# Kernel optimization log

Measured on AMD Instinct MI355X. Metric: run time of the kernel, lower is better.

The kernel has to match this reference:

```python
import jax, jax.numpy as jnp
import numpy as np

B, N, D = 4, 256, 128
HID = 128
IN_DIM = 4 * D + 4  # h_i, h_j, |h_i-h_j|, h_i*h_j + 2 base + 2 completion feats


def setup_inputs() -> dict:
    key = jax.random.key(0)
    k1, k2, k3, k4, k5, k6, k7 = jax.random.split(key, 7)
    node_latents = jax.random.normal(k1, (B, N, D), dtype=jnp.float32)
    base_edge_logits = jax.random.normal(k2, (B, N, N), dtype=jnp.float32)
    completion_logits = jax.random.normal(k3, (B, N, N), dtype=jnp.float32)
    # MLP params (build_mlp: Linear(in,hid) -> ReLU -> Linear(hid,1) for num_layers=2)
    s1 = 1.0 / np.sqrt(IN_DIM)
    s2 = 1.0 / np.sqrt(HID)
    W1 = jax.random.uniform(k4, (IN_DIM, HID), minval=-s1, maxval=s1, dtype=jnp.float32)
    b1 = jax.random.uniform(k5, (HID,), minval=-s1, maxval=s1, dtype=jnp.float32)
    W2 = jax.random.uniform(k6, (HID, 1), minval=-s2, maxval=s2, dtype=jnp.float32)
    b2 = jax.random.uniform(k7, (1,), minval=-s2, maxval=s2, dtype=jnp.float32)
    return {"node_latents": node_latents, "base_edge_logits": base_edge_logits,
            "completion_logits": completion_logits, "W1": W1, "b1": b1, "W2": W2, "b2": b2}


def reference(node_latents, base_edge_logits, completion_logits, W1, b1, W2, b2):
    bsz, num_nodes, hidden_dim = node_latents.shape
    h_i = jnp.broadcast_to(node_latents[:, :, None, :], (bsz, num_nodes, num_nodes, hidden_dim))
    h_j = jnp.broadcast_to(node_latents[:, None, :, :], (bsz, num_nodes, num_nodes, hidden_dim))
    base = jnp.clip(base_edge_logits, -20.0, 20.0)
    comp = jnp.clip(completion_logits, -20.0, 20.0)
    pair_feat = jnp.concatenate([
        h_i, h_j, jnp.abs(h_i - h_j), h_i * h_j,
        base[..., None], jax.nn.sigmoid(base)[..., None],
        comp[..., None], jax.nn.sigmoid(comp)[..., None],
    ], axis=-1)  # [B, N, N, IN_DIM]
    hdn = jax.nn.relu(jnp.einsum('bijf,fh->bijh', pair_feat, W1) + b1)
    logits = (jnp.einsum('bijh,ho->bijo', hdn, W2) + b2)[..., 0]  # [B, N, N]
    logits = 0.5 * (logits + jnp.swapaxes(logits, 1, 2))
    diag = jnp.eye(num_nodes, dtype=bool)[None]
    return jnp.where(diag, jnp.float32(-1e9), logits)
```

## Files before the change

kernel.cpp:

```cpp
#include <hip/hip_runtime.h>
#include <cstdint>


typedef float f32x4 __attribute__((ext_vector_type(4)));
typedef short bf16x8 __attribute__((ext_vector_type(8)));

#define INV256 0.00390625f

__device__ __forceinline__ uint32_t pk4(float a, float b, float c, float d) {
  uint32_t u = __builtin_amdgcn_cvt_pk_fp8_f32(a, b, 0, false);
  u = __builtin_amdgcn_cvt_pk_fp8_f32(c, d, u, true);
  return u;
}
__device__ __forceinline__ uint32_t pkbf2(float lo, float hi) {
  uint32_t l = __builtin_bit_cast(uint32_t, lo);
  uint32_t h = __builtin_bit_cast(uint32_t, hi);
  return (l >> 16) | (h & 0xffff0000u);
}
__device__ __forceinline__ uint32_t rnebf(float x) {
  uint32_t u = __builtin_bit_cast(uint32_t, x);
  return (u + 0x7fffu + ((u >> 16) & 1u)) >> 16;
}
__device__ __forceinline__ uint32_t pkbf2r(float lo, float hi) {
  return rnebf(lo) | (rnebf(hi) << 16);
}
__device__ __forceinline__ float ulo(uint32_t u) {
  return __builtin_bit_cast(float, u << 16);
}
__device__ __forceinline__ float uhi(uint32_t u) {
  return __builtin_bit_cast(float, u & 0xffff0000u);
}
__device__ __forceinline__ long mk64(uint32_t lo, uint32_t hi) {
  return (long)((((unsigned long long)hi) << 32) | lo);
}
__device__ __forceinline__ bf16x8 mkbf8(uint32_t a, uint32_t b, uint32_t c, uint32_t d) {
  uint4 u;
  u.x = a; u.y = b; u.z = c; u.w = d;
  return __builtin_bit_cast(bf16x8, u);
}

__global__ __launch_bounds__(128) void pre_k(const float* __restrict__ node,
                                             const float* __restrict__ W1,
                                             const float* __restrict__ b1,
                                             float* __restrict__ PiB,
                                             float* __restrict__ Pjf,
                                             uint32_t* __restrict__ W1f8) {
  int bid = blockIdx.x;
  int tid = threadIdx.x;
  if (bid < 32) {
    int ks = bid >> 2, nip = (bid >> 1) & 1, wn = bid & 1;
    int lane = tid & 63, nilow = tid >> 6;
    int quad = lane >> 4, col = lane & 15;
    int h = wn * 64 + (nip * 2 + nilow) * 16 + col;
    int k0 = ks * 32 + quad * 8;
    float w[8];
#pragma unroll
    for (int t = 0; t < 8; ++t) w[t] = W1[(256 + k0 + t) * 128 + h] * 256.0f;
    uint2 u;
    u.x = pk4(w[0], w[1], w[2], w[3]);
    u.y = pk4(w[4], w[5], w[6], w[7]);
    reinterpret_cast<uint2*>(W1f8)[(bid * 64 + lane) * 2 + nilow] = u;
  } else {
    __shared__ float sN[128];
    int row = bid - 32;
    int h = tid;
    sN[h] = node[row * 128 + h];
    __syncthreads();
    float ai = 0.f, aj = 0.f;
#pragma unroll 8
    for (int d = 0; d < 128; ++d) {
      float v = sN[d];
      ai = fmaf(v, W1[d * 128 + h], ai);
      aj = fmaf(v, W1[(128 + d) * 128 + h], aj);
    }
    PiB[row * 128 + h] = 256.0f * (ai + b1[h]);
    Pjf[row * 128 + h] = 256.0f * aj;
  }
}

__global__ __launch_bounds__(256, 5) void main_k(
    const float* __restrict__ node, const float* __restrict__ baseL,
    const float* __restrict__ compL, const float* __restrict__ W1,
    const float* __restrict__ W2, const float* __restrict__ b2,
    const uint32_t* __restrict__ W1f8, const float* __restrict__ PiB,
    const float* __restrict__ Pjf, float* __restrict__ out) {
  __shared__ __align__(16) char smem[16384 + 8448 + 1024];
  char* sF = smem;
  uint32_t* sPP = reinterpret_cast<uint32_t*>(smem + 16384);
  uint4* sScal = reinterpret_cast<uint4*>(smem + 16384 + 8448);
  float* sP = reinterpret_cast<float*>(smem);

  const int tid = threadIdx.x;
  const int bx = blockIdx.x;
  const int b = bx / 528;
  const int t = bx - b * 528;
  int tI = (int)((65.0f - sqrtf(4225.0f - 8.0f * (float)t)) * 0.5f);
  tI = (tI < 0) ? 0 : (tI > 31 ? 31 : tI);
  while (((65 * tI - tI * tI) >> 1) > t) --tI;
  while (tI < 31 && ((65 * (tI + 1) - (tI + 1) * (tI + 1)) >> 1) <= t) ++tI;
  const int tJ = tI + (t - ((65 * tI - tI * tI) >> 1));
  const int I0 = tI * 8, J0 = tJ * 8;
  const int rowB = b * 256;

  const int lane = tid & 63;
  const int wn2 = tid >> 6;
  const int col = lane & 15, quad = lane >> 4;

  const int uB = ((wn2 & 1) << 1) | (wn2 >> 1);
  uint4 gB[8];
#pragma unroll
  for (int ks = 0; ks < 8; ++ks)
    gB[ks] = reinterpret_cast<const uint4*>(W1f8)[(ks * 4 + uB) * 64 + lane];

#pragma unroll
  for (int it = 0; it < 2; ++it) {
    int fidx = it * 256 + tid;
    int row = fidx >> 5, d4 = fidx & 31;
    int gr = rowB + ((row < 8) ? (I0 + row) : (J0 + row - 8));
    float4 a = reinterpret_cast<const float4*>(PiB + (size_t)gr * 128)[d4];
    float4 c = reinterpret_cast<const float4*>(Pjf + (size_t)gr * 128)[d4];
    uint4 u;
    u.x = pkbf2(a.x, c.x);
    u.y = pkbf2(a.y, c.y);
    u.z = pkbf2(a.z, c.z);
    u.w = pkbf2(a.w, c.w);
    *reinterpret_cast<uint4*>(&sPP[row * 132 + d4 * 4]) = u;
  }

  if (tid < 128) {
    int p = tid & 63, dir = tid >> 6;
    int iN = I0 + (p >> 3), jN = J0 + (p & 7);
    int rr = dir ? jN : iN, cc = dir ? iN : jN;
    float bl = fminf(fmaxf(baseL[(size_t)(rowB + rr) * 256 + cc], -20.f), 20.f);
    float cl = fminf(fmaxf(compL[(size_t)(rowB + rr) * 256 + cc], -20.f), 20.f);
    uint2 u;
    u.x = pkbf2(256.f * bl, 256.f / (1.f + __expf(-bl)));
    u.y = pkbf2(256.f * cl, 256.f / (1.f + __expf(-cl)));
    *reinterpret_cast<uint2*>(reinterpret_cast<char*>(&sScal[p]) + dir * 8) = u;
  }

  float cW2[2];
  bf16x8 Bf[2];
#pragma unroll
  for (int ni = 0; ni < 2; ++ni) {
    int h = (wn2 * 2 + ni) * 16 + col;
    uint32_t w01 = pkbf2r(W1[512 * 128 + h], W1[513 * 128 + h]);
    uint32_t w23 = pkbf2r(W1[514 * 128 + h], W1[515 * 128 + h]);
    Bf[ni] = mkbf8(quad == 0 ? w01 : 0u, quad == 0 ? w23 : 0u, 0u, 0u);
    cW2[ni] = W2[h] * INV256;
  }
  const float b2v = b2[0];

  {
    const int d4 = tid & 31;
    const int rr = tid >> 5;
    const int ks1 = d4 >> 3, qd = (d4 >> 1) & 3, kb = (d4 & 1) * 4;
    const int scolbase = 2 * qd + 4 * ks1;
    const float4 hj = *reinterpret_cast<const float4*>(node + (size_t)(rowB + J0 + rr) * 128 + d4 * 4);
#pragma unroll
    for (int ii = 0; ii < 8; ++ii) {
      const float4 hi = *reinterpret_cast<const float4*>(node + (size_t)(rowB + I0 + ii) * 128 + d4 * 4);
      uint32_t du = pk4(fabsf(hi.x - hj.x), fabsf(hi.y - hj.y),
                        fabsf(hi.z - hj.z), fabsf(hi.w - hj.w));
      uint32_t pu = pk4(hi.x * hj.x, hi.y * hj.y, hi.z * hj.z, hi.w * hj.w);
      int p = ii * 8 + rr;
      int colp = p & 15, mi = p >> 4;
      int scol = (colp + scolbase) & 15;
      uint32_t addr = mi * 512 + qd * 128 + scol * 8 + kb;
      *reinterpret_cast<uint32_t*>(sF + ks1 * 2048 + addr) = du;
      *reinterpret_cast<uint32_t*>(sF + (ks1 + 4) * 2048 + addr) = pu;
    }
  }
  __syncthreads();

  f32x4 acc[4][2] = {};
#pragma unroll
  for (int ks = 0; ks < 8; ++ks) {
    long bb0 = mk64(gB[ks].x, gB[ks].y);
    long bb1 = mk64(gB[ks].z, gB[ks].w);
    const int ascol = (col + 2 * quad + 4 * (ks & 3)) & 15;
    const char* aks = sF + ks * 2048 + quad * 128 + ascol * 8;
#pragma unroll
    for (int mi = 0; mi < 4; ++mi) {
      uint2 av = *reinterpret_cast<const uint2*>(aks + mi * 512);
      long aa = mk64(av.x, av.y);
      acc[mi][0] = __builtin_amdgcn_mfma_f32_16x16x32_fp8_fp8(aa, bb0, acc[mi][0], 0, 0, 0);
      acc[mi][1] = __builtin_amdgcn_mfma_f32_16x16x32_fp8_fp8(aa, bb1, acc[mi][1], 0, 0, 0);
    }
  }
  __syncthreads();

  uint32_t uJ[4][2];
#pragma unroll
  for (int r = 0; r < 4; ++r)
#pragma unroll
    for (int ni = 0; ni < 2; ++ni)
      uJ[r][ni] = sPP[(8 + (quad & 1) * 4 + r) * 132 + (wn2 * 2 + ni) * 16 + col];

  const f32x4 zf = {};
#pragma unroll
  for (int mi = 0; mi < 4; ++mi) {
    const int ii = mi * 2 + (quad >> 1);
    uint32_t uI[2];
#pragma unroll
    for (int ni = 0; ni < 2; ++ni)
      uI[ni] = sPP[ii * 132 + (wn2 * 2 + ni) * 16 + col];

    uint4 sc4 = sScal[mi * 16 + col];
    bf16x8 af = mkbf8(quad == 0 ? sc4.x : 0u, quad == 0 ? sc4.y : 0u, 0u, 0u);
    bf16x8 am = mkbf8(quad == 0 ? sc4.z : 0u, quad == 0 ? sc4.w : 0u, 0u, 0u);
    f32x4 SF[2], SM[2];
#pragma unroll
    for (int ni = 0; ni < 2; ++ni) {
      SF[ni] = __builtin_amdgcn_mfma_f32_16x16x32_bf16(af, Bf[ni], zf, 0, 0, 0);
      SM[ni] = __builtin_amdgcn_mfma_f32_16x16x32_bf16(am, Bf[ni], zf, 0, 0, 0);
    }

#pragma unroll
    for (int r = 0; r < 4; ++r) {
      int p = mi * 16 + quad * 4 + r;
      float vf = 0.f, vm = 0.f;
#pragma unroll
      for (int ni = 0; ni < 2; ++ni) {
        float piI = ulo(uI[ni]), pjI = uhi(uI[ni]);
        float piJ = ulo(uJ[r][ni]), pjJ = uhi(uJ[r][ni]);
        float a = acc[mi][ni][r];
        float pf = ((a + SF[ni][r]) + piI) + pjJ;
        float pm = ((a + SM[ni][r]) + piJ) + pjI;
        vf = fmaf(fmaxf(pf, 0.f), cW2[ni], vf);
        vm = fmaf(fmaxf(pm, 0.f), cW2[ni], vm);
      }
      vf += __shfl_xor(vf, 1);
      vf += __shfl_xor(vf, 2);
      vm += __shfl_xor(vm, 1);
      vm += __shfl_xor(vm, 2);
      if ((col & 3) == 0) {
        int part = wn2 * 4 + (col >> 2);
        sP[p * 40 + part] = vf;
        sP[p * 40 + 20 + part] = vm;
      }
    }
  }
  __syncthreads();

  if (tid < 64) {
    int p = tid;
    const float4* pf4 = reinterpret_cast<const float4*>(sP + p * 40);
    const float4* pm4 = reinterpret_cast<const float4*>(sP + p * 40 + 20);
    float4 fa = pf4[0], fb = pf4[1], fc = pf4[2], fd = pf4[3];
    float4 ma = pm4[0], mb = pm4[1], mc = pm4[2], md = pm4[3];
    float sumF = (fa.x + fa.y + fa.z + fa.w) + (fb.x + fb.y + fb.z + fb.w) +
                 (fc.x + fc.y + fc.z + fc.w) + (fd.x + fd.y + fd.z + fd.w);
    float sumM = (ma.x + ma.y + ma.z + ma.w) + (mb.x + mb.y + mb.z + mb.w) +
                 (mc.x + mc.y + mc.z + mc.w) + (md.x + md.y + md.z + md.w);
    float val = 0.5f * (sumF + sumM) + b2v;
    int iN = I0 + (p >> 3), jN = J0 + (p & 7);
    if (iN == jN) val = -1e9f;
    out[(size_t)(rowB + iN) * 256 + jN] = val;
    out[(size_t)(rowB + jN) * 256 + iN] = val;
  }
}

extern "C" void kernel_launch(void* const* d_in, const int* in_sizes, int n_in,
                              void* d_out, int out_size, void* d_ws, size_t ws_size,
                              hipStream_t stream) {
  const float* node = (const float*)d_in[0];
  const float* baseL = (const float*)d_in[1];
  const float* compL = (const float*)d_in[2];
  const float* W1 = (const float*)d_in[3];
  const float* b1 = (const float*)d_in[4];
  const float* W2 = (const float*)d_in[5];
  const float* b2 = (const float*)d_in[6];
  float* out = (float*)d_out;

  char* ws = (char*)d_ws;
  float* PiB = (float*)(ws);
  float* Pjf = (float*)(ws + (512 << 10));
  uint32_t* W1f8 = (uint32_t*)(ws + (1024 << 10));

  pre_k<<<1056, 128, 0, stream>>>(node, W1, b1, PiB, Pjf, W1f8);
  main_k<<<2112, 256, 0, stream>>>(node, baseL, compL, W1, W2, b2, W1f8, PiB, Pjf, out);
}
```

Baseline: 92.91 us.

## Compute node projections with bf16 MFMA and pre-pack them for main kernel

```diff
diff --git a/kernel.cpp b/kernel.cpp
--- a/kernel.cpp
+++ b/kernel.cpp
@@ -39,42 +39,75 @@
   return __builtin_bit_cast(bf16x8, u);
 }
 
-__global__ __launch_bounds__(128) void pre_k(const float* __restrict__ node,
+__global__ __launch_bounds__(256) void pre_k(const float* __restrict__ node,
                                              const float* __restrict__ W1,
                                              const float* __restrict__ b1,
-                                             float* __restrict__ PiB,
-                                             float* __restrict__ Pjf,
+                                             uint32_t* __restrict__ Ppk,
                                              uint32_t* __restrict__ W1f8) {
   int bid = blockIdx.x;
   int tid = threadIdx.x;
   if (bid < 32) {
-    int ks = bid >> 2, nip = (bid >> 1) & 1, wn = bid & 1;
-    int lane = tid & 63, nilow = tid >> 6;
-    int quad = lane >> 4, col = lane & 15;
-    int h = wn * 64 + (nip * 2 + nilow) * 16 + col;
-    int k0 = ks * 32 + quad * 8;
-    float w[8];
-#pragma unroll
-    for (int t = 0; t < 8; ++t) w[t] = W1[(256 + k0 + t) * 128 + h] * 256.0f;
-    uint2 u;
-    u.x = pk4(w[0], w[1], w[2], w[3]);
-    u.y = pk4(w[4], w[5], w[6], w[7]);
-    reinterpret_cast<uint2*>(W1f8)[(bid * 64 + lane) * 2 + nilow] = u;
-  } else {
-    __shared__ float sN[128];
-    int row = bid - 32;
-    int h = tid;
-    sN[h] = node[row * 128 + h];
-    __syncthreads();
-    float ai = 0.f, aj = 0.f;
-#pragma unroll 8
-    for (int d = 0; d < 128; ++d) {
-      float v = sN[d];
-      ai = fmaf(v, W1[d * 128 + h], ai);
-      aj = fmaf(v, W1[(128 + d) * 128 + h], aj);
-    }
-    PiB[row * 128 + h] = 256.0f * (ai + b1[h]);
-    Pjf[row * 128 + h] = 256.0f * aj;
+    if (tid < 128) {
+      int ks = bid >> 2, nip = (bid >> 1) & 1, wn = bid & 1;
+      int lane = tid & 63, nilow = tid >> 6;
+      int quad = lane >> 4, col = lane & 15;
+      int h = wn * 64 + (nip * 2 + nilow) * 16 + col;
+      int k0 = ks * 32 + quad * 8;
+      float w[8];
+#pragma unroll
+      for (int t = 0; t < 8; ++t) w[t] = W1[(256 + k0 + t) * 128 + h] * 256.0f;
+      uint2 u;
+      u.x = pk4(w[0], w[1], w[2], w[3]);
+      u.y = pk4(w[4], w[5], w[6], w[7]);
+      reinterpret_cast<uint2*>(W1f8)[(bid * 64 + lane) * 2 + nilow] = u;
+    }
+    return;
+  }
+  __shared__ float sC[16 * 264];
+  const int gb = bid - 32;
+  const int gr0 = gb * 16;
+  const int w = tid >> 6, lane = tid & 63, col = lane & 15, quad = lane >> 4;
+
+  bf16x8 Af[4];
+  const float* arow = node + (size_t)(gr0 + col) * 128 + quad * 8;
+#pragma unroll
+  for (int ks = 0; ks < 4; ++ks) {
+    float4 a0 = *reinterpret_cast<const float4*>(arow + ks * 32);
+    float4 a1 = *reinterpret_cast<const float4*>(arow + ks * 32 + 4);
+    Af[ks] = mkbf8(pkbf2r(a0.x, a0.y), pkbf2r(a0.z, a0.w),
+                   pkbf2r(a1.x, a1.y), pkbf2r(a1.z, a1.w));
+  }
+  const int colbase = w * 64;
+  const float* wbase = W1 + (size_t)((w >> 1) * 128) * 128;
+#pragma unroll
+  for (int ni = 0; ni < 4; ++ni) {
+    const int hh = (colbase + ni * 16 + col) & 127;
+    f32x4 acc = {};
+#pragma unroll
+    for (int ks = 0; ks < 4; ++ks) {
+      const float* wp = wbase + (size_t)(ks * 32 + quad * 8) * 128 + hh;
+      bf16x8 Bf = mkbf8(pkbf2r(wp[0], wp[128]), pkbf2r(wp[256], wp[384]),
+                        pkbf2r(wp[512], wp[640]), pkbf2r(wp[768], wp[896]));
+      acc = __builtin_amdgcn_mfma_f32_16x16x32_bf16(Af[ks], Bf, acc, 0, 0, 0);
+    }
+#pragma unroll
+    for (int r = 0; r < 4; ++r)
+      sC[(quad * 4 + r) * 264 + colbase + ni * 16 + col] = acc[r];
+  }
+  __syncthreads();
+  {
+    const int row = tid >> 4, hq = tid & 15;
+    uint32_t ov[8];
+#pragma unroll
+    for (int hh = 0; hh < 8; ++hh) {
+      int h = hq * 8 + hh;
+      float pib = 256.f * (sC[row * 264 + h] + b1[h]);
+      float pjf = 256.f * sC[row * 264 + 128 + h];
+      ov[hh] = pkbf2r(pib, pjf);
+    }
+    uint4* dst = reinterpret_cast<uint4*>(Ppk + (size_t)(gr0 + row) * 128 + hq * 8);
+    dst[0] = *reinterpret_cast<uint4*>(&ov[0]);
+    dst[1] = *reinterpret_cast<uint4*>(&ov[4]);
   }
 }
 
@@ -82,8 +115,8 @@
     const float* __restrict__ node, const float* __restrict__ baseL,
     const float* __restrict__ compL, const float* __restrict__ W1,
     const float* __restrict__ W2, const float* __restrict__ b2,
-    const uint32_t* __restrict__ W1f8, const float* __restrict__ PiB,
-    const float* __restrict__ Pjf, float* __restrict__ out) {
+    const uint32_t* __restrict__ W1f8, const uint32_t* __restrict__ Ppk,
+    float* __restrict__ out) {
   __shared__ __align__(16) char smem[16384 + 8448 + 1024];
   char* sF = smem;
   uint32_t* sPP = reinterpret_cast<uint32_t*>(smem + 16384);
@@ -115,16 +148,10 @@
 #pragma unroll
   for (int it = 0; it < 2; ++it) {
     int fidx = it * 256 + tid;
-    int row = fidx >> 5, d4 = fidx & 31;
+    int row = fidx >> 5, q = fidx & 31;
     int gr = rowB + ((row < 8) ? (I0 + row) : (J0 + row - 8));
-    float4 a = reinterpret_cast<const float4*>(PiB + (size_t)gr * 128)[d4];
-    float4 c = reinterpret_cast<const float4*>(Pjf + (size_t)gr * 128)[d4];
-    uint4 u;
-    u.x = pkbf2(a.x, c.x);
-    u.y = pkbf2(a.y, c.y);
-    u.z = pkbf2(a.z, c.z);
-    u.w = pkbf2(a.w, c.w);
-    *reinterpret_cast<uint4*>(&sPP[row * 132 + d4 * 4]) = u;
+    uint4 u = reinterpret_cast<const uint4*>(Ppk + (size_t)gr * 128)[q];
+    *reinterpret_cast<uint4*>(&sPP[row * 132 + q * 4]) = u;
   }
 
   if (tid < 128) {
@@ -274,10 +301,9 @@
   float* out = (float*)d_out;
 
   char* ws = (char*)d_ws;
-  float* PiB = (float*)(ws);
-  float* Pjf = (float*)(ws + (512 << 10));
-  uint32_t* W1f8 = (uint32_t*)(ws + (1024 << 10));
-
-  pre_k<<<1056, 128, 0, stream>>>(node, W1, b1, PiB, Pjf, W1f8);
-  main_k<<<2112, 256, 0, stream>>>(node, baseL, compL, W1, W2, b2, W1f8, PiB, Pjf, out);
-}
+  uint32_t* Ppk = (uint32_t*)ws;
+  uint32_t* W1f8 = (uint32_t*)(ws + (512 << 10));
+
+  pre_k<<<96, 256, 0, stream>>>(node, W1, b1, Ppk, W1f8);
+  main_k<<<2112, 256, 0, stream>>>(node, baseL, compL, W1, W2, b2, W1f8, Ppk, out);
+}
```

Measured after the change: 89.77 us. 3.4% less time.
